# Performance work log

Hardware: AMD Instinct MI355X
Metric: run time of the kernel (lower is better)

Reference implementation:

```python
import jax, jax.numpy as jnp
import numpy as np

DIM = 128
KERNEL = 7
NUM_HEADS = 4
HEAD_DIM = DIM // NUM_HEADS
SCALE = HEAD_DIM ** (-0.5)


def _nbhd_indices(size, k):
    # NATTEN edge-clamped neighborhood: start index so the k-window stays in bounds
    pos = jnp.arange(size)
    start = jnp.clip(pos - k // 2, 0, size - k)          # (size,)
    idx = start[:, None] + jnp.arange(k)[None, :]        # (size, k) absolute key index
    bias = idx - pos[:, None] + (k - 1)                  # (size, k) rpb index in [0, 2k-2]
    return idx, bias


def setup_inputs() -> dict:
    key = jax.random.key(0)
    ks = jax.random.split(key, 6)
    B, H, W = 4, 64, 64
    x = jax.random.normal(ks[0], (B, H, W, DIM), dtype=jnp.float32)
    w_qkv = jax.random.normal(ks[1], (DIM, 3 * DIM), dtype=jnp.float32) * (DIM ** -0.5)
    b_qkv = jax.random.normal(ks[2], (3 * DIM,), dtype=jnp.float32) * 0.02
    rpb = jax.random.normal(ks[3], (NUM_HEADS, 2 * KERNEL - 1, 2 * KERNEL - 1), dtype=jnp.float32) * 0.02
    w_proj = jax.random.normal(ks[4], (DIM, DIM), dtype=jnp.float32) * (DIM ** -0.5)
    b_proj = jax.random.normal(ks[5], (DIM,), dtype=jnp.float32) * 0.02
    return {"x": x, "w_qkv": w_qkv, "b_qkv": b_qkv, "rpb": rpb,
            "w_proj": w_proj, "b_proj": b_proj}


def reference(x, w_qkv, b_qkv, rpb, w_proj, b_proj):
    B, H, W, C = x.shape
    k = KERNEL
    # qkv projection; split order (3, heads, head_dim) matches torch reshape
    qkv = (x @ w_qkv + b_qkv).reshape(B, H, W, 3, NUM_HEADS, HEAD_DIM)
    q = jnp.transpose(qkv[..., 0, :, :], (0, 3, 1, 2, 4)) * SCALE  # (B,nh,H,W,hd)
    kk = jnp.transpose(qkv[..., 1, :, :], (0, 3, 1, 2, 4))
    v = jnp.transpose(qkv[..., 2, :, :], (0, 3, 1, 2, 4))

    idx_i, bias_i = _nbhd_indices(H, k)  # (H,k)
    idx_j, bias_j = _nbhd_indices(W, k)  # (W,k)

    # gather local k x k neighborhoods of keys/values: (B,nh,H,W,k,k,hd)
    II = idx_i[:, None, :, None]
    JJ = idx_j[None, :, None, :]
    k_nb = kk[:, :, II, JJ, :]
    v_nb = v[:, :, II, JJ, :]

    # QK + relative position bias gathered per offset
    attn = jnp.einsum('bnhwd,bnhwpqd->bnhwpq', q, k_nb)
    attn = attn + rpb[:, bias_i[:, None, :, None], bias_j[None, :, None, :]][None]

    # softmax over the k*k neighborhood
    attn = jax.nn.softmax(attn.reshape(B, NUM_HEADS, H, W, k * k), axis=-1)
    attn = attn.reshape(B, NUM_HEADS, H, W, k, k)

    out = jnp.einsum('bnhwpq,bnhwpqd->bnhwd', attn, v_nb)
    out = jnp.transpose(out, (0, 2, 3, 1, 4)).reshape(B, H, W, C)
    return out @ w_proj + b_proj
```

## Files before the change

### kernel.cpp

```cpp
#include <hip/hip_runtime.h>
#include <hip/hip_bf16.h>

typedef float f4 __attribute__((ext_vector_type(4)));
typedef float f32x4 __attribute__((ext_vector_type(4)));
typedef unsigned short u16x8 __attribute__((ext_vector_type(8)));
typedef short short8 __attribute__((ext_vector_type(8)));

#define QSCALE 0.17677669529663689f

__device__ inline float b2f(unsigned short u){
  union{unsigned int i; float f;} z; z.i = ((unsigned int)u)<<16; return z.f;
}
__device__ inline unsigned short f2b(float f){
  union{float f; unsigned int i;} z; z.f=f;
  unsigned int i = z.i;
  return (unsigned short)((i + 0x7FFFu + ((i>>16)&1u)) >> 16);
}

__global__ __launch_bounds__(256) void k_prep(const float* __restrict__ wq,
    const float* __restrict__ wp, unsigned short* __restrict__ wT,
    unsigned short* __restrict__ wpT)
{
  __shared__ float T[32][129];
  const int b = blockIdx.x, t = threadIdx.x;
  const float* src; unsigned short* dst; int N, n0;
  if (b < 12){ src = wq; dst = wT;  N = 384; n0 = b*32; }
  else       { src = wp; dst = wpT; N = 128; n0 = (b-12)*32; }
  for (int i = t; i < 4096; i += 256){
    int k = i >> 5, c = i & 31;
    T[c][k] = src[k*N + n0 + c];
  }
  __syncthreads();
  const int n = t >> 3, k0 = (t & 7) << 4;
#pragma unroll
  for (int e = 0; e < 2; ++e){
    u16x8 o;
#pragma unroll
    for (int j = 0; j < 8; ++j) o[j] = f2b(T[n][k0 + e*8 + j]);
    *(u16x8*)&dst[(n0+n)*128 + k0 + e*8] = o;
  }
}

__global__ __launch_bounds__(256) void k_qkv_mfma(const float* __restrict__ x,
    const unsigned short* __restrict__ wT, const float* __restrict__ bias,
    unsigned short* __restrict__ qo, unsigned short* __restrict__ ko,
    unsigned short* __restrict__ vo)
{
  __shared__ short lds[64*128 + 128*128];
  short* As = lds;
  short* Bs = lds + 64*128;
  const int t = threadIdx.x;
  const int m0 = blockIdx.x * 64;
  const int ny = blockIdx.y;
  const int n0 = ny * 128;

  for (int c = t; c < 1024; c += 256){
    int row = c >> 4, k0 = (c & 15) << 3;
    const float* p = &x[(m0+row)*128 + k0];
    f4 lo = *(const f4*)p, hi = *(const f4*)(p+4);
    u16x8 v;
    v[0]=f2b(lo[0]); v[1]=f2b(lo[1]); v[2]=f2b(lo[2]); v[3]=f2b(lo[3]);
    v[4]=f2b(hi[0]); v[5]=f2b(hi[1]); v[6]=f2b(hi[2]); v[7]=f2b(hi[3]);
    int byte = (row<<8) + (k0<<1);
    *(u16x8*)((char*)As + (byte ^ ((row&7)<<4))) = v;
  }
  for (int c = t; c < 2048; c += 256){
    int n = c >> 4, k0 = (c & 15) << 3;
    u16x8 v = *(const u16x8*)&wT[(n0+n)*128 + k0];
    int byte = (n<<8) + (k0<<1);
    *(u16x8*)((char*)Bs + (byte ^ ((n&7)<<4))) = v;
  }
  __syncthreads();

  const int w = t >> 6, l = t & 63;
  const int wm = (w >> 1) * 32, wn = (w & 1) * 64;
  const int lr = l & 15, lk = (l >> 4) << 3;
  f32x4 acc[2][4] = {};
#pragma unroll
  for (int k0 = 0; k0 < 128; k0 += 32){
    const int koff = k0 + lk;
    short8 a[2], bf[4];
#pragma unroll
    for (int fm = 0; fm < 2; ++fm){
      int row = wm + fm*16 + lr;
      int byte = (row<<8) + (koff<<1);
      a[fm] = *(short8*)((char*)As + (byte ^ ((row&7)<<4)));
    }
#pragma unroll
    for (int fn = 0; fn < 4; ++fn){
      int rn = wn + fn*16 + lr;
      int byte = (rn<<8) + (koff<<1);
      bf[fn] = *(short8*)((char*)Bs + (byte ^ ((rn&7)<<4)));
    }
#pragma unroll
    for (int fm = 0; fm < 2; ++fm)
#pragma unroll
      for (int fn = 0; fn < 4; ++fn)
        acc[fm][fn] = __builtin_amdgcn_mfma_f32_16x16x32_bf16(a[fm], bf[fn], acc[fm][fn], 0, 0, 0);
  }
  __syncthreads();

  unsigned short* C = (unsigned short*)lds;
  const float scale = (ny == 0) ? QSCALE : 1.0f;
#pragma unroll
  for (int fm = 0; fm < 2; ++fm)
#pragma unroll
    for (int fn = 0; fn < 4; ++fn){
      int col = wn + fn*16 + lr;
      float bv = bias[n0 + col];
#pragma unroll
      for (int r = 0; r < 4; ++r){
        int row = wm + fm*16 + ((l>>4)<<2) + r;
        C[row*136 + col] = f2b((acc[fm][fn][r] + bv) * scale);
      }
    }
  __syncthreads();
  unsigned short* dst = ny==0 ? qo : (ny==1 ? ko : vo);
  for (int c = t; c < 1024; c += 256){
    int row = c >> 4, k0 = (c & 15) << 3;
    int head = k0 >> 5, d0 = k0 & 31;
    *(u16x8*)&dst[(head*16384 + m0 + row)*32 + d0] = *(u16x8*)&C[row*136 + k0];
  }
}

__global__ __launch_bounds__(256) void k_attn(
    const unsigned short* __restrict__ qg,
    const unsigned short* __restrict__ kg,
    const unsigned short* __restrict__ vg,
    const float* __restrict__ rpb,
    unsigned short* __restrict__ ao)
{
  __shared__ unsigned short ks[196*40];
  __shared__ unsigned short vs[196*40];
  __shared__ float rs[169];
  const int t = threadIdx.x;
  const int b = blockIdx.z >> 2, h = blockIdx.z & 3;
  const int th0 = blockIdx.y * 8, tw0 = blockIdx.x * 8;
  const int bi0 = min(max(th0-3,0),50);
  const int bj0 = min(max(tw0-3,0),50);
  const unsigned short* kb = kg + (h*16384 + b*4096)*32;
  const unsigned short* vb = vg + (h*16384 + b*4096)*32;

  for (int c = t; c < 784; c += 256){
    int tok = c >> 2, ch = c & 3;
    int trow = tok/14, tcol = tok - trow*14;
    int g = ((bi0+trow)*64 + (bj0+tcol))*32 + ch*8;
    int lo = tok*40 + ch*8;
    *(u16x8*)&ks[lo] = *(const u16x8*)&kb[g];
    *(u16x8*)&vs[lo] = *(const u16x8*)&vb[g];
  }
  for (int c = t; c < 169; c += 256) rs[c] = rpb[h*169 + c];
  __syncthreads();

  const int lt = t >> 2, p = t & 3;
  const int ti = th0 + (lt >> 3), tj = tw0 + (lt & 7);
  const int si = min(max(ti-3,0),57), sj = min(max(tj-3,0),57);
  const int li = si - bi0, lj = sj - bj0;
  const int ri = si - ti + 6, rj = sj - tj + 6;

  float q[32];
  {
    int qb = (h*16384 + b*4096 + ti*64 + tj)*32;
#pragma unroll
    for (int j=0;j<4;++j){
      u16x8 u = *(const u16x8*)&qg[qb + j*8];
#pragma unroll
      for (int e=0;e<8;++e) q[j*8+e] = b2f(u[e]);
    }
  }

  float s[13]; int toks[13];
  float mx = -1e30f;
#pragma unroll
  for (int it = 0; it < 13; ++it){
    int n = p + (it << 2);
    bool ok = (n < 49);
    int nn = ok ? n : 48;
    int pi = nn / 7, pj = nn - pi*7;
    int tok = (li+pi)*14 + (lj+pj);
    toks[it] = tok;
    float acc = rs[(ri+pi)*13 + (rj+pj)];
#pragma unroll
    for (int j=0;j<4;++j){
      u16x8 kk = *(const u16x8*)&ks[tok*40 + j*8];
#pragma unroll
      for (int e=0;e<8;++e) acc += q[j*8+e]*b2f(kk[e]);
    }
    s[it] = ok ? acc : -1e30f;
    mx = fmaxf(mx, s[it]);
  }
  mx = fmaxf(mx, __shfl_xor(mx, 1));
  mx = fmaxf(mx, __shfl_xor(mx, 2));

  float l = 0.f, o[32];
#pragma unroll
  for (int d=0; d<32; ++d) o[d] = 0.f;
#pragma unroll
  for (int it = 0; it < 13; ++it){
    float e = __expf(s[it] - mx);
    l += e;
    int tok = toks[it];
#pragma unroll
    for (int j=0;j<4;++j){
      u16x8 vv = *(const u16x8*)&vs[tok*40 + j*8];
#pragma unroll
      for (int e2=0;e2<8;++e2) o[j*8+e2] += e*b2f(vv[e2]);
    }
  }
  l += __shfl_xor(l, 1);
  l += __shfl_xor(l, 2);
#pragma unroll
  for (int d=0; d<32; ++d) o[d] += __shfl_xor(o[d], 1);
#pragma unroll
  for (int d=0; d<32; ++d) o[d] += __shfl_xor(o[d], 2);

  float inv = 1.f / l;
  int ob = (b*4096 + ti*64 + tj)*128 + h*32 + p*8;
  u16x8 w8;
#pragma unroll
  for (int e=0;e<8;++e) w8[e] = f2b(o[p*8+e]*inv);
  *(u16x8*)&ao[ob] = w8;
}

__global__ __launch_bounds__(256) void k_proj_mfma(
    const unsigned short* __restrict__ a,
    const unsigned short* __restrict__ wpT, const float* __restrict__ bias,
    float* __restrict__ out)
{
  __shared__ short lds[64*128 + 128*128];
  short* As = lds;
  short* Bs = lds + 64*128;
  const int t = threadIdx.x;
  const int m0 = blockIdx.x * 64;

  for (int c = t; c < 1024; c += 256){
    int row = c >> 4, k0 = (c & 15) << 3;
    u16x8 v = *(const u16x8*)&a[(m0+row)*128 + k0];
    int byte = (row<<8) + (k0<<1);
    *(u16x8*)((char*)As + (byte ^ ((row&7)<<4))) = v;
  }
  for (int c = t; c < 2048; c += 256){
    int n = c >> 4, k0 = (c & 15) << 3;
    u16x8 v = *(const u16x8*)&wpT[n*128 + k0];
    int byte = (n<<8) + (k0<<1);
    *(u16x8*)((char*)Bs + (byte ^ ((n&7)<<4))) = v;
  }
  __syncthreads();

  const int w = t >> 6, l = t & 63;
  const int wm = (w >> 1) * 32, wn = (w & 1) * 64;
  const int lr = l & 15, lk = (l >> 4) << 3;
  f32x4 acc[2][4] = {};
#pragma unroll
  for (int k0 = 0; k0 < 128; k0 += 32){
    const int koff = k0 + lk;
    short8 afr[2], bf[4];
#pragma unroll
    for (int fm = 0; fm < 2; ++fm){
      int row = wm + fm*16 + lr;
      int byte = (row<<8) + (koff<<1);
      afr[fm] = *(short8*)((char*)As + (byte ^ ((row&7)<<4)));
    }
#pragma unroll
    for (int fn = 0; fn < 4; ++fn){
      int rn = wn + fn*16 + lr;
      int byte = (rn<<8) + (koff<<1);
      bf[fn] = *(short8*)((char*)Bs + (byte ^ ((rn&7)<<4)));
    }
#pragma unroll
    for (int fm = 0; fm < 2; ++fm)
#pragma unroll
      for (int fn = 0; fn < 4; ++fn)
        acc[fm][fn] = __builtin_amdgcn_mfma_f32_16x16x32_bf16(afr[fm], bf[fn], acc[fm][fn], 0, 0, 0);
  }
  __syncthreads();

  float* C = (float*)lds;
#pragma unroll
  for (int fm = 0; fm < 2; ++fm)
#pragma unroll
    for (int fn = 0; fn < 4; ++fn){
      int col = wn + fn*16 + lr;
      float bv = bias[col];
#pragma unroll
      for (int r = 0; r < 4; ++r){
        int row = wm + fm*16 + ((l>>4)<<2) + r;
        C[row*132 + col] = acc[fm][fn][r] + bv;
      }
    }
  __syncthreads();
  for (int c = t; c < 2048; c += 256){
    int row = c >> 5, k0 = (c & 31) << 2;
    *(f4*)&out[(m0+row)*128 + k0] = *(const f4*)&C[row*132 + k0];
  }
}

extern "C" void kernel_launch(void* const* d_in, const int* in_sizes, int n_in,
                              void* d_out, int out_size, void* d_ws, size_t ws_size,
                              hipStream_t stream) {
  const float* x      = (const float*)d_in[0];
  const float* w_qkv  = (const float*)d_in[1];
  const float* b_qkv  = (const float*)d_in[2];
  const float* rpb    = (const float*)d_in[3];
  const float* w_proj = (const float*)d_in[4];
  const float* b_proj = (const float*)d_in[5];
  float* out = (float*)d_out;

  unsigned short* qo  = (unsigned short*)d_ws;
  unsigned short* ko  = qo + 16384*128;
  unsigned short* vo  = ko + 16384*128;
  unsigned short* ao  = vo + 16384*128;
  unsigned short* wT  = ao + 16384*128;
  unsigned short* wpT = wT + 384*128;

  k_prep<<<16, 256, 0, stream>>>(w_qkv, w_proj, wT, wpT);
  k_qkv_mfma<<<dim3(256, 3), 256, 0, stream>>>(x, wT, b_qkv, qo, ko, vo);
  k_attn<<<dim3(8, 8, 16), 256, 0, stream>>>(qo, ko, vo, rpb, ao);
  k_proj_mfma<<<256, 256, 0, stream>>>(ao, wpT, b_proj, out);
}
```

Measured before the change: 52.22 us.

## Fuse weight transpose/bf16 conversion into GEMM loads, split proj grid, hoist Q load

Drops the separate k_prep launch. The QKV and projection GEMM kernels now read fp32 weights directly, then convert and transpose them into swizzled LDS themselves. The projection kernel is split along N into two 64-column halves, doubling the grid and halving its LDS use. The attention kernel issues its Q global loads before the K/V tile staging so the two overlap. The cost is redundant weight conversion in every block and wider fp32 weight reads.

```diff
diff --git a/kernel.cpp b/kernel.cpp
--- a/kernel.cpp
+++ b/kernel.cpp
@@ -5,6 +5,7 @@
 typedef float f32x4 __attribute__((ext_vector_type(4)));
 typedef unsigned short u16x8 __attribute__((ext_vector_type(8)));
 typedef short short8 __attribute__((ext_vector_type(8)));
+typedef unsigned int uint2v __attribute__((ext_vector_type(2)));
 
 #define QSCALE 0.17677669529663689f
 
@@ -17,32 +18,8 @@
   return (unsigned short)((i + 0x7FFFu + ((i>>16)&1u)) >> 16);
 }
 
-__global__ __launch_bounds__(256) void k_prep(const float* __restrict__ wq,
-    const float* __restrict__ wp, unsigned short* __restrict__ wT,
-    unsigned short* __restrict__ wpT)
-{
-  __shared__ float T[32][129];
-  const int b = blockIdx.x, t = threadIdx.x;
-  const float* src; unsigned short* dst; int N, n0;
-  if (b < 12){ src = wq; dst = wT;  N = 384; n0 = b*32; }
-  else       { src = wp; dst = wpT; N = 128; n0 = (b-12)*32; }
-  for (int i = t; i < 4096; i += 256){
-    int k = i >> 5, c = i & 31;
-    T[c][k] = src[k*N + n0 + c];
-  }
-  __syncthreads();
-  const int n = t >> 3, k0 = (t & 7) << 4;
-#pragma unroll
-  for (int e = 0; e < 2; ++e){
-    u16x8 o;
-#pragma unroll
-    for (int j = 0; j < 8; ++j) o[j] = f2b(T[n][k0 + e*8 + j]);
-    *(u16x8*)&dst[(n0+n)*128 + k0 + e*8] = o;
-  }
-}
-
 __global__ __launch_bounds__(256) void k_qkv_mfma(const float* __restrict__ x,
-    const unsigned short* __restrict__ wT, const float* __restrict__ bias,
+    const float* __restrict__ w, const float* __restrict__ bias,
     unsigned short* __restrict__ qo, unsigned short* __restrict__ ko,
     unsigned short* __restrict__ vo)
 {
@@ -64,16 +41,27 @@
     int byte = (row<<8) + (k0<<1);
     *(u16x8*)((char*)As + (byte ^ ((row&7)<<4))) = v;
   }
-  for (int c = t; c < 2048; c += 256){
-    int n = c >> 4, k0 = (c & 15) << 3;
-    u16x8 v = *(const u16x8*)&wT[(n0+n)*128 + k0];
-    int byte = (n<<8) + (k0<<1);
-    *(u16x8*)((char*)Bs + (byte ^ ((n&7)<<4))) = v;
-  }
-  __syncthreads();
-
-  const int w = t >> 6, l = t & 63;
-  const int wm = (w >> 1) * 32, wn = (w & 1) * 64;
+  for (int c = t; c < 1024; c += 256){
+    int kb = c >> 5, nb = c & 31;
+    const float* p = &w[(kb*4)*384 + n0 + nb*4];
+    f4 r0 = *(const f4*)p;
+    f4 r1 = *(const f4*)(p + 384);
+    f4 r2 = *(const f4*)(p + 768);
+    f4 r3 = *(const f4*)(p + 1152);
+#pragma unroll
+    for (int j = 0; j < 4; ++j){
+      int n = nb*4 + j;
+      uint2v val;
+      val[0] = (unsigned int)f2b(r0[j]) | ((unsigned int)f2b(r1[j])<<16);
+      val[1] = (unsigned int)f2b(r2[j]) | ((unsigned int)f2b(r3[j])<<16);
+      int byte = (n<<8) + (kb<<3);
+      *(uint2v*)((char*)Bs + (byte ^ ((n&7)<<4))) = val;
+    }
+  }
+  __syncthreads();
+
+  const int wv = t >> 6, l = t & 63;
+  const int wm = (wv >> 1) * 32, wn = (wv & 1) * 64;
   const int lr = l & 15, lk = (l >> 4) << 3;
   f32x4 acc[2][4] = {};
 #pragma unroll
@@ -141,6 +129,19 @@
   const unsigned short* kb = kg + (h*16384 + b*4096)*32;
   const unsigned short* vb = vg + (h*16384 + b*4096)*32;
 
+  const int lt = t >> 2, p = t & 3;
+  const int ti = th0 + (lt >> 3), tj = tw0 + (lt & 7);
+  float q[32];
+  {
+    int qb = (h*16384 + b*4096 + ti*64 + tj)*32;
+#pragma unroll
+    for (int j=0;j<4;++j){
+      u16x8 u = *(const u16x8*)&qg[qb + j*8];
+#pragma unroll
+      for (int e=0;e<8;++e) q[j*8+e] = b2f(u[e]);
+    }
+  }
+
   for (int c = t; c < 784; c += 256){
     int tok = c >> 2, ch = c & 3;
     int trow = tok/14, tcol = tok - trow*14;
@@ -152,22 +153,9 @@
   for (int c = t; c < 169; c += 256) rs[c] = rpb[h*169 + c];
   __syncthreads();
 
-  const int lt = t >> 2, p = t & 3;
-  const int ti = th0 + (lt >> 3), tj = tw0 + (lt & 7);
   const int si = min(max(ti-3,0),57), sj = min(max(tj-3,0),57);
   const int li = si - bi0, lj = sj - bj0;
   const int ri = si - ti + 6, rj = sj - tj + 6;
-
-  float q[32];
-  {
-    int qb = (h*16384 + b*4096 + ti*64 + tj)*32;
-#pragma unroll
-    for (int j=0;j<4;++j){
-      u16x8 u = *(const u16x8*)&qg[qb + j*8];
-#pragma unroll
-      for (int e=0;e<8;++e) q[j*8+e] = b2f(u[e]);
-    }
-  }
 
   float s[13]; int toks[13];
   float mx = -1e30f;
@@ -224,14 +212,15 @@
 
 __global__ __launch_bounds__(256) void k_proj_mfma(
     const unsigned short* __restrict__ a,
-    const unsigned short* __restrict__ wpT, const float* __restrict__ bias,
+    const float* __restrict__ w, const float* __restrict__ bias,
     float* __restrict__ out)
 {
-  __shared__ short lds[64*128 + 128*128];
+  __shared__ short lds[64*128 + 64*128];
   short* As = lds;
   short* Bs = lds + 64*128;
   const int t = threadIdx.x;
   const int m0 = blockIdx.x * 64;
+  const int n0 = blockIdx.y * 64;
 
   for (int c = t; c < 1024; c += 256){
     int row = c >> 4, k0 = (c & 15) << 3;
@@ -239,22 +228,33 @@
     int byte = (row<<8) + (k0<<1);
     *(u16x8*)((char*)As + (byte ^ ((row&7)<<4))) = v;
   }
-  for (int c = t; c < 2048; c += 256){
-    int n = c >> 4, k0 = (c & 15) << 3;
-    u16x8 v = *(const u16x8*)&wpT[n*128 + k0];
-    int byte = (n<<8) + (k0<<1);
-    *(u16x8*)((char*)Bs + (byte ^ ((n&7)<<4))) = v;
-  }
-  __syncthreads();
-
-  const int w = t >> 6, l = t & 63;
-  const int wm = (w >> 1) * 32, wn = (w & 1) * 64;
+  for (int c = t; c < 512; c += 256){
+    int kb = c >> 4, nb = c & 15;
+    const float* p = &w[(kb*4)*128 + n0 + nb*4];
+    f4 r0 = *(const f4*)p;
+    f4 r1 = *(const f4*)(p + 128);
+    f4 r2 = *(const f4*)(p + 256);
+    f4 r3 = *(const f4*)(p + 384);
+#pragma unroll
+    for (int j = 0; j < 4; ++j){
+      int n = nb*4 + j;
+      uint2v val;
+      val[0] = (unsigned int)f2b(r0[j]) | ((unsigned int)f2b(r1[j])<<16);
+      val[1] = (unsigned int)f2b(r2[j]) | ((unsigned int)f2b(r3[j])<<16);
+      int byte = (n<<8) + (kb<<3);
+      *(uint2v*)((char*)Bs + (byte ^ ((n&7)<<4))) = val;
+    }
+  }
+  __syncthreads();
+
+  const int wv = t >> 6, l = t & 63;
+  const int wm = (wv >> 1) * 32, wn = (wv & 1) * 32;
   const int lr = l & 15, lk = (l >> 4) << 3;
-  f32x4 acc[2][4] = {};
+  f32x4 acc[2][2] = {};
 #pragma unroll
   for (int k0 = 0; k0 < 128; k0 += 32){
     const int koff = k0 + lk;
-    short8 afr[2], bf[4];
+    short8 afr[2], bf[2];
 #pragma unroll
     for (int fm = 0; fm < 2; ++fm){
       int row = wm + fm*16 + lr;
@@ -262,7 +262,7 @@
       afr[fm] = *(short8*)((char*)As + (byte ^ ((row&7)<<4)));
     }
 #pragma unroll
-    for (int fn = 0; fn < 4; ++fn){
+    for (int fn = 0; fn < 2; ++fn){
       int rn = wn + fn*16 + lr;
       int byte = (rn<<8) + (koff<<1);
       bf[fn] = *(short8*)((char*)Bs + (byte ^ ((rn&7)<<4)));
@@ -270,7 +270,7 @@
 #pragma unroll
     for (int fm = 0; fm < 2; ++fm)
 #pragma unroll
-      for (int fn = 0; fn < 4; ++fn)
+      for (int fn = 0; fn < 2; ++fn)
         acc[fm][fn] = __builtin_amdgcn_mfma_f32_16x16x32_bf16(afr[fm], bf[fn], acc[fm][fn], 0, 0, 0);
   }
   __syncthreads();
@@ -279,19 +279,19 @@
 #pragma unroll
   for (int fm = 0; fm < 2; ++fm)
 #pragma unroll
-    for (int fn = 0; fn < 4; ++fn){
+    for (int fn = 0; fn < 2; ++fn){
       int col = wn + fn*16 + lr;
-      float bv = bias[col];
+      float bv = bias[n0 + col];
 #pragma unroll
       for (int r = 0; r < 4; ++r){
         int row = wm + fm*16 + ((l>>4)<<2) + r;
-        C[row*132 + col] = acc[fm][fn][r] + bv;
+        C[row*68 + col] = acc[fm][fn][r] + bv;
       }
     }
   __syncthreads();
-  for (int c = t; c < 2048; c += 256){
-    int row = c >> 5, k0 = (c & 31) << 2;
-    *(f4*)&out[(m0+row)*128 + k0] = *(const f4*)&C[row*132 + k0];
+  for (int c = t; c < 1024; c += 256){
+    int row = c >> 4, colc = (c & 15) << 2;
+    *(f4*)&out[(m0+row)*128 + n0 + colc] = *(const f4*)&C[row*68 + colc];
   }
 }
 
@@ -310,11 +310,8 @@
   unsigned short* ko  = qo + 16384*128;
   unsigned short* vo  = ko + 16384*128;
   unsigned short* ao  = vo + 16384*128;
-  unsigned short* wT  = ao + 16384*128;
-  unsigned short* wpT = wT + 384*128;
-
-  k_prep<<<16, 256, 0, stream>>>(w_qkv, w_proj, wT, wpT);
-  k_qkv_mfma<<<dim3(256, 3), 256, 0, stream>>>(x, wT, b_qkv, qo, ko, vo);
+
+  k_qkv_mfma<<<dim3(256, 3), 256, 0, stream>>>(x, w_qkv, b_qkv, qo, ko, vo);
   k_attn<<<dim3(8, 8, 16), 256, 0, stream>>>(qo, ko, vo, rpb, ao);
-  k_proj_mfma<<<256, 256, 0, stream>>>(ao, wpT, b_proj, out);
-}
+  k_proj_mfma<<<dim3(256, 2), 256, 0, stream>>>(ao, w_proj, b_proj, out);
+}
```

Result: faster. 45.42 us (-13.0%).
